# Performance work log

Hardware: AMD Instinct MI355X
Metric: run time of the kernel (lower is better)

The kernel has to match this reference:

```python
import jax, jax.numpy as jnp
import numpy as np

N_NODES = 100000
N_EDGES = 640000
IN_D = 128
OUT_D = 128


def setup_inputs() -> dict:
    key = jax.random.key(0)
    k_x, k_ei, k_ws, k_wn = jax.random.split(key, 4)
    scale = 1.0 / np.sqrt(IN_D)
    return {
        "x": jax.random.normal(k_x, (N_NODES, IN_D), dtype=jnp.float32),
        "ei": jax.random.randint(k_ei, (2, N_EDGES), 0, N_NODES, dtype=jnp.int64),
        "Ws": jax.random.normal(k_ws, (IN_D, OUT_D), dtype=jnp.float32) * scale,
        "bs": jnp.zeros((OUT_D,), dtype=jnp.float32),
        "Wn": jax.random.normal(k_wn, (IN_D, OUT_D), dtype=jnp.float32) * scale,
        "bn": jnp.zeros((OUT_D,), dtype=jnp.float32),
    }


def reference(x, ei, Ws, bs, Wn, bn):
    # x: [N, in_d], ei: [2, E]
    src, dst = ei[0], ei[1]
    n = x.shape[0]
    # scatter-sum of gathered source features onto destinations
    agg = jax.ops.segment_sum(x[src], dst, num_segments=n)  # [N, in_d]
    # in-degree per destination node
    deg = jax.ops.segment_sum(jnp.ones(src.shape[0], dtype=x.dtype), dst, num_segments=n)  # [N]
    agg = agg / jnp.maximum(deg, 1.0)[:, None]
    # dual linear + relu (dropout is identity in eval)
    return jax.nn.relu(x @ Ws + bs + agg @ Wn + bn)
```

## Files before the change

### kernel.cpp

```cpp
#include <hip/hip_runtime.h>
#include <hip/hip_bf16.h>

#define D 128

typedef __attribute__((ext_vector_type(8))) short short8v;
typedef __attribute__((ext_vector_type(4))) float f32x4;

__device__ __forceinline__ short f2bf(float f) {
    union { float f; unsigned u; } v;
    v.f = f;
    unsigned u = v.u;
    unsigned r = (u + 0x7FFFu + ((u >> 16) & 1u)) >> 16;
    return (short)r;
}

__device__ __forceinline__ float bf2f(unsigned u16) {
    union { unsigned u; float f; } v;
    v.u = u16 << 16;
    return v.f;
}

__device__ __forceinline__ unsigned pkbf2(float lo, float hi) {
    __hip_bfloat162 h = __float22bfloat162_rn(make_float2(lo, hi));
    union { __hip_bfloat162 h; unsigned u; } v;
    v.h = h;
    return v.u;
}

__global__ __launch_bounds__(256) void prep_kernel(const int* __restrict__ dst,
                                                   int* __restrict__ counts, int nE,
                                                   const float* __restrict__ Ws,
                                                   const float* __restrict__ Wn,
                                                   short* __restrict__ WT2,
                                                   const float* __restrict__ x,
                                                   unsigned short* __restrict__ xb,
                                                   int nElem) {
    const int nbE = (nE + 255) >> 8;
    const int b = blockIdx.x;
    if (b < nbE) {
        int e = b * 256 + threadIdx.x;
        if (e < nE) atomicAdd(&counts[dst[e]], 1);
    } else if (b < nbE + 128) {
        int idx = (b - nbE) * 256 + threadIdx.x;
        int nn = idx >> 8;
        int k = idx & 255;
        float v = (k < D) ? Ws[k * D + nn] : Wn[(k - D) * D + nn];
        WT2[idx] = f2bf(v);
    } else {
        int idx = (b - nbE - 128) * 256 + threadIdx.x;
        int base = idx * 8;
        if (base < nElem) {
            float4 lo = *reinterpret_cast<const float4*>(x + base);
            float4 hi = *reinterpret_cast<const float4*>(x + base + 4);
            union { short8v s8; unsigned u[4]; } p;
            p.u[0] = pkbf2(lo.x, lo.y);
            p.u[1] = pkbf2(lo.z, lo.w);
            p.u[2] = pkbf2(hi.x, hi.y);
            p.u[3] = pkbf2(hi.z, hi.w);
            *reinterpret_cast<short8v*>(xb + base) = p.s8;
        }
    }
}

__global__ __launch_bounds__(256) void scan_fused_kernel(int* __restrict__ counts,
                                                         int* __restrict__ bsums,
                                                         int* __restrict__ done,
                                                         int* __restrict__ rowptr,
                                                         int n, int nb) {
    __shared__ int sh[256];
    __shared__ int red[8];
    const int b = blockIdx.x;
    const int t = threadIdx.x;
    const int i0 = b * 1024 + t * 4;
    int c[4];
    int s = 0;
#pragma unroll
    for (int j = 0; j < 4; ++j) {
        c[j] = (i0 + j < n) ? counts[i0 + j] : 0;
        s += c[j];
    }
    sh[t] = s;
    __syncthreads();
    for (int off = 1; off < 256; off <<= 1) {
        int u = (t >= off) ? sh[t - off] : 0;
        __syncthreads();
        sh[t] += u;
        __syncthreads();
    }
    if (t == 0) {
        bsums[b] = sh[255];
        __threadfence();
        atomicAdd(done, 1);
        while (atomicAdd(done, 0) < nb) { }
    }
    __syncthreads();
    int xv = (t < nb) ? atomicAdd(&bsums[t], 0) : 0;
    int vb = (t < b) ? xv : 0;
#pragma unroll
    for (int off = 32; off > 0; off >>= 1) {
        vb += __shfl_down(vb, off, 64);
        xv += __shfl_down(xv, off, 64);
    }
    if ((t & 63) == 0) { red[t >> 6] = vb; red[4 + (t >> 6)] = xv; }
    __syncthreads();
    const int base = red[0] + red[1] + red[2] + red[3];
    const int total = red[4] + red[5] + red[6] + red[7];
    int run = base + sh[t] - s;
#pragma unroll
    for (int j = 0; j < 4; ++j) {
        int i = i0 + j;
        if (i < n) {
            rowptr[i] = run;
            counts[i] = run;
            run += c[j];
        }
    }
    if (b == nb - 1 && t == 0) rowptr[n] = total;
}

__global__ __launch_bounds__(256) void fill_kernel(const int* __restrict__ src,
                                                   const int* __restrict__ dst,
                                                   int* __restrict__ cursor,
                                                   int* __restrict__ csr, int nE) {
    int e = blockIdx.x * 256 + threadIdx.x;
    if (e < nE) {
        int pos = atomicAdd(&cursor[dst[e]], 1);
        csr[pos] = src[e];
    }
}

__global__ __launch_bounds__(256) void gather_kernel(const int* __restrict__ rowptr,
                                                     const int* __restrict__ csr,
                                                     const unsigned short* __restrict__ xb,
                                                     unsigned* __restrict__ aggOut,
                                                     int aggStride, int n) {
    const int wave = threadIdx.x >> 6;
    const int lane = threadIdx.x & 63;
    const int d0 = blockIdx.x * 8 + wave * 2;
    if (d0 >= n) return;
    const bool has1 = (d0 + 1) < n;

    const int begA = rowptr[d0];
    const int endA = rowptr[d0 + 1];
    const int begB = has1 ? endA : 0;
    const int endB = has1 ? rowptr[d0 + 2] : 0;
    const int ofs = lane * 2;
    float ax0 = 0.f, ay0 = 0.f, ax1 = 0.f, ay1 = 0.f;
    int iA = begA, iB = begB;

#define GLD(sidx) (*reinterpret_cast<const unsigned*>(xb + (size_t)(sidx) * D + ofs))
    while (iA + 4 <= endA && iB + 4 <= endB) {
        int a0 = csr[iA], a1 = csr[iA + 1], a2 = csr[iA + 2], a3 = csr[iA + 3];
        int b0 = csr[iB], b1 = csr[iB + 1], b2 = csr[iB + 2], b3 = csr[iB + 3];
        unsigned va0 = GLD(a0), va1 = GLD(a1), va2 = GLD(a2), va3 = GLD(a3);
        unsigned vb0 = GLD(b0), vb1 = GLD(b1), vb2 = GLD(b2), vb3 = GLD(b3);
        ax0 += (bf2f(va0 & 0xffffu) + bf2f(va1 & 0xffffu)) +
               (bf2f(va2 & 0xffffu) + bf2f(va3 & 0xffffu));
        ay0 += (bf2f(va0 >> 16) + bf2f(va1 >> 16)) + (bf2f(va2 >> 16) + bf2f(va3 >> 16));
        ax1 += (bf2f(vb0 & 0xffffu) + bf2f(vb1 & 0xffffu)) +
               (bf2f(vb2 & 0xffffu) + bf2f(vb3 & 0xffffu));
        ay1 += (bf2f(vb0 >> 16) + bf2f(vb1 >> 16)) + (bf2f(vb2 >> 16) + bf2f(vb3 >> 16));
        iA += 4;
        iB += 4;
    }
    while (iA + 4 <= endA) {
        int a0 = csr[iA], a1 = csr[iA + 1], a2 = csr[iA + 2], a3 = csr[iA + 3];
        unsigned va0 = GLD(a0), va1 = GLD(a1), va2 = GLD(a2), va3 = GLD(a3);
        ax0 += (bf2f(va0 & 0xffffu) + bf2f(va1 & 0xffffu)) +
               (bf2f(va2 & 0xffffu) + bf2f(va3 & 0xffffu));
        ay0 += (bf2f(va0 >> 16) + bf2f(va1 >> 16)) + (bf2f(va2 >> 16) + bf2f(va3 >> 16));
        iA += 4;
    }
    while (iB + 4 <= endB) {
        int b0 = csr[iB], b1 = csr[iB + 1], b2 = csr[iB + 2], b3 = csr[iB + 3];
        unsigned vb0 = GLD(b0), vb1 = GLD(b1), vb2 = GLD(b2), vb3 = GLD(b3);
        ax1 += (bf2f(vb0 & 0xffffu) + bf2f(vb1 & 0xffffu)) +
               (bf2f(vb2 & 0xffffu) + bf2f(vb3 & 0xffffu));
        ay1 += (bf2f(vb0 >> 16) + bf2f(vb1 >> 16)) + (bf2f(vb2 >> 16) + bf2f(vb3 >> 16));
        iB += 4;
    }
    while (iA < endA) {
        unsigned v = GLD(csr[iA]);
        ax0 += bf2f(v & 0xffffu);
        ay0 += bf2f(v >> 16);
        ++iA;
    }
    while (iB < endB) {
        unsigned v = GLD(csr[iB]);
        ax1 += bf2f(v & 0xffffu);
        ay1 += bf2f(v >> 16);
        ++iB;
    }
#undef GLD

    const float invA = 1.0f / fmaxf((float)(endA - begA), 1.0f);
    aggOut[(size_t)d0 * aggStride + lane] = pkbf2(ax0 * invA, ay0 * invA);
    if (has1) {
        const float invB = 1.0f / fmaxf((float)(endB - begB), 1.0f);
        aggOut[(size_t)(d0 + 1) * aggStride + lane] = pkbf2(ax1 * invB, ay1 * invB);
    }
}

template <bool INPLACE>
__global__ __launch_bounds__(256) void gemm_kernel(const unsigned short* __restrict__ xb,
                                                   const short* __restrict__ WT2,
                                                   const float* __restrict__ bs,
                                                   const float* __restrict__ bn,
                                                   const unsigned* aggIn, int aggStride,
                                                   float* __restrict__ out, int nStrips) {
    const int wave = threadIdx.x >> 6;
    const int lane = threadIdx.x & 63;
    const int lrow = lane & 15;
    const int q = lane >> 4;
    const int ko = q * 8;

    short8v b[2][8];
#pragma unroll
    for (int j = 0; j < 2; ++j) {
        const short* __restrict__ wp = WT2 + (size_t)((wave * 2 + j) * 16 + lrow) * 256 + ko;
#pragma unroll
        for (int ks = 0; ks < 8; ++ks)
            b[j][ks] = *reinterpret_cast<const short8v*>(wp + ks * 32);
    }
    float4 bias[2];
#pragma unroll
    for (int j = 0; j < 2; ++j) {
        const int cb = (wave * 2 + j) * 16 + q * 4;
        float4 v1 = *reinterpret_cast<const float4*>(bs + cb);
        float4 v2 = *reinterpret_cast<const float4*>(bn + cb);
        bias[j] = make_float4(v1.x + v2.x, v1.y + v2.y, v1.z + v2.z, v1.w + v2.w);
    }

    const int stride = gridDim.x;

    auto loadA = [&](int strip, short8v* ax, uint4* ag) {
        const unsigned short* __restrict__ xr = xb + (size_t)(strip * 16 + lrow) * D + ko;
        const unsigned* __restrict__ ar = aggIn + (size_t)(strip * 16 + lrow) * aggStride;
#pragma unroll
        for (int ks = 0; ks < 4; ++ks) {
            ax[ks] = *reinterpret_cast<const short8v*>(xr + ks * 32);
            ag[ks] = *reinterpret_cast<const uint4*>(ar + q * 4 + ks * 16);
        }
    };

    auto compute = [&](int strip, const short8v* ax, const uint4* ag) {
        f32x4 acc[2];
        acc[0] = (f32x4){0.f, 0.f, 0.f, 0.f};
        acc[1] = (f32x4){0.f, 0.f, 0.f, 0.f};
#pragma unroll
        for (int j = 0; j < 2; ++j) {
#pragma unroll
            for (int ks = 0; ks < 4; ++ks) {
                union { uint4 u4; short8v s8; } cv;
                cv.u4 = ag[ks];
                acc[j] = __builtin_amdgcn_mfma_f32_16x16x32_bf16(b[j][ks], ax[ks], acc[j], 0, 0, 0);
                acc[j] = __builtin_amdgcn_mfma_f32_16x16x32_bf16(b[j][ks + 4], cv.s8, acc[j], 0, 0, 0);
            }
        }
        if (INPLACE) __syncthreads();
        const size_t rb = (size_t)(strip * 16 + lrow) * D;
#pragma unroll
        for (int j = 0; j < 2; ++j) {
            const int cb = (wave * 2 + j) * 16 + q * 4;
            float4 o;
            o.x = fmaxf(acc[j][0] + bias[j].x, 0.f);
            o.y = fmaxf(acc[j][1] + bias[j].y, 0.f);
            o.z = fmaxf(acc[j][2] + bias[j].z, 0.f);
            o.w = fmaxf(acc[j][3] + bias[j].w, 0.f);
            *reinterpret_cast<float4*>(out + rb + cb) = o;
        }
    };

    short8v axA[4], axB[4];
    uint4 agA[4], agB[4];
    int strip = blockIdx.x;
    if (strip >= nStrips) return;
    loadA(strip, axA, agA);
    for (; strip < nStrips; strip += 2 * stride) {
        const int s1 = strip + stride;
        if (s1 < nStrips) loadA(s1, axB, agB);
        compute(strip, axA, agA);
        if (s1 < nStrips) {
            const int s2 = s1 + stride;
            if (s2 < nStrips) loadA(s2, axA, agA);
            compute(s1, axB, agB);
        }
    }
}

extern "C" void kernel_launch(void* const* d_in, const int* in_sizes, int n_in,
                              void* d_out, int out_size, void* d_ws, size_t ws_size,
                              hipStream_t stream) {
    const float* x  = (const float*)d_in[0];
    const int*   ei = (const int*)d_in[1];
    const float* Ws = (const float*)d_in[2];
    const float* bs = (const float*)d_in[3];
    const float* Wn = (const float*)d_in[4];
    const float* bn = (const float*)d_in[5];
    float* out = (float*)d_out;

    const int n  = in_sizes[0] / D;
    const int nE = in_sizes[1] / 2;
    const int* src = ei;
    const int* dst = ei + nE;
    const int nb = (n + 1023) / 1024;
    const int nElem = n * D;

    char* w = (char*)d_ws;
    unsigned short* xb = (unsigned short*)w;  w += (size_t)nElem * 2;
    short* WT2   = (short*)w;                 w += (size_t)256 * D * 2;
    int* counts  = (int*)w;                   w += (size_t)n * 4;
    int* bsums   = (int*)w;                   w += 128 * 4;
    int* done    = (int*)w;                   w += 16;
    int* rowptr  = (int*)w;                   w += (size_t)(n + 1) * 4;
    int* csr     = (int*)w;                   w += (size_t)nE * 4;
    size_t off = (size_t)(w - (char*)d_ws);
    off = (off + 15) & ~(size_t)15;
    unsigned short* aggb = (unsigned short*)((char*)d_ws + off);
    const bool sep = (off + (size_t)nElem * 2) <= ws_size;

    const int nbE = (nE + 255) / 256;
    const int nXb = (nElem / 8 + 255) / 256;

    hipMemsetAsync(counts, 0, (size_t)(n + 128 + 4) * sizeof(int), stream);
    prep_kernel<<<nbE + 128 + nXb, 256, 0, stream>>>(dst, counts, nE, Ws, Wn, WT2, x, xb, nElem);
    scan_fused_kernel<<<nb, 256, 0, stream>>>(counts, bsums, done, rowptr, n, nb);
    fill_kernel<<<(nE + 255) / 256, 256, 0, stream>>>(src, dst, counts, csr, nE);

    unsigned* aggPtr = sep ? (unsigned*)aggb : (unsigned*)out;
    const int aggStride = sep ? (D / 2) : D;
    gather_kernel<<<(n + 7) / 8, 256, 0, stream>>>(rowptr, csr, xb, aggPtr, aggStride, n);

    const int nStrips = (n + 15) / 16;
    if (sep)
        gemm_kernel<false><<<2048, 256, 0, stream>>>(xb, WT2, bs, bn, (const unsigned*)aggb,
                                                     aggStride, out, nStrips);
    else
        gemm_kernel<true><<<2048, 256, 0, stream>>>(xb, WT2, bs, bn, (const unsigned*)out,
                                                    aggStride, out, nStrips);
}
```

Measured before the change: 163.2 us.

## Fuse CSR fill into scan kernel via grid barrier, nontemporal output, fewer GEMM blocks

Merges the fill kernel into the scan kernel using a spin-wait grid barrier on the done counter, removing one launch and its dependency gap. The fill loop is grid-strided over the scan's roughly 98 blocks, so it has much less parallelism than the old fill launch. The GEMM epilogue now uses nontemporal stores to avoid polluting the cache with output, and the GEMM grid is halved. The spin barrier assumes all scan blocks are co-resident, which holds at this block count.

```diff
diff --git a/kernel.cpp b/kernel.cpp
--- a/kernel.cpp
+++ b/kernel.cpp
@@ -62,11 +62,14 @@
     }
 }
 
-__global__ __launch_bounds__(256) void scan_fused_kernel(int* __restrict__ counts,
-                                                         int* __restrict__ bsums,
-                                                         int* __restrict__ done,
-                                                         int* __restrict__ rowptr,
-                                                         int n, int nb) {
+__global__ __launch_bounds__(256) void scan_fill_kernel(int* __restrict__ counts,
+                                                        int* __restrict__ bsums,
+                                                        int* __restrict__ done,
+                                                        int* __restrict__ rowptr,
+                                                        const int* __restrict__ src,
+                                                        const int* __restrict__ dst,
+                                                        int* __restrict__ csr, int nE,
+                                                        int n, int nb) {
     __shared__ int sh[256];
     __shared__ int red[8];
     const int b = blockIdx.x;
@@ -111,20 +114,22 @@
         int i = i0 + j;
         if (i < n) {
             rowptr[i] = run;
-            counts[i] = run;
+            atomicExch(&counts[i], run);
             run += c[j];
         }
     }
     if (b == nb - 1 && t == 0) rowptr[n] = total;
-}
-
-__global__ __launch_bounds__(256) void fill_kernel(const int* __restrict__ src,
-                                                   const int* __restrict__ dst,
-                                                   int* __restrict__ cursor,
-                                                   int* __restrict__ csr, int nE) {
-    int e = blockIdx.x * 256 + threadIdx.x;
-    if (e < nE) {
-        int pos = atomicAdd(&cursor[dst[e]], 1);
+
+    __syncthreads();
+    if (t == 0) {
+        atomicAdd(done, 1);
+        while (atomicAdd(done, 0) < 2 * nb) { }
+    }
+    __syncthreads();
+
+    const int gsz = nb * 256;
+    for (int e = b * 256 + t; e < nE; e += gsz) {
+        int pos = atomicAdd(&counts[dst[e]], 1);
         csr[pos] = src[e];
     }
 }
@@ -262,12 +267,12 @@
 #pragma unroll
         for (int j = 0; j < 2; ++j) {
             const int cb = (wave * 2 + j) * 16 + q * 4;
-            float4 o;
-            o.x = fmaxf(acc[j][0] + bias[j].x, 0.f);
-            o.y = fmaxf(acc[j][1] + bias[j].y, 0.f);
-            o.z = fmaxf(acc[j][2] + bias[j].z, 0.f);
-            o.w = fmaxf(acc[j][3] + bias[j].w, 0.f);
-            *reinterpret_cast<float4*>(out + rb + cb) = o;
+            f32x4 o;
+            o[0] = fmaxf(acc[j][0] + bias[j].x, 0.f);
+            o[1] = fmaxf(acc[j][1] + bias[j].y, 0.f);
+            o[2] = fmaxf(acc[j][2] + bias[j].z, 0.f);
+            o[3] = fmaxf(acc[j][3] + bias[j].w, 0.f);
+            __builtin_nontemporal_store(o, reinterpret_cast<f32x4*>(out + rb + cb));
         }
     };
 
@@ -322,10 +327,9 @@
     const int nbE = (nE + 255) / 256;
     const int nXb = (nElem / 8 + 255) / 256;
 
-    hipMemsetAsync(counts, 0, (size_t)(n + 128 + 4) * sizeof(int), stream);
+    (void)hipMemsetAsync(counts, 0, (size_t)(n + 128 + 4) * sizeof(int), stream);
     prep_kernel<<<nbE + 128 + nXb, 256, 0, stream>>>(dst, counts, nE, Ws, Wn, WT2, x, xb, nElem);
-    scan_fused_kernel<<<nb, 256, 0, stream>>>(counts, bsums, done, rowptr, n, nb);
-    fill_kernel<<<(nE + 255) / 256, 256, 0, stream>>>(src, dst, counts, csr, nE);
+    scan_fill_kernel<<<nb, 256, 0, stream>>>(counts, bsums, done, rowptr, src, dst, csr, nE, n, nb);
 
     unsigned* aggPtr = sep ? (unsigned*)aggb : (unsigned*)out;
     const int aggStride = sep ? (D / 2) : D;
@@ -333,9 +337,9 @@
 
     const int nStrips = (n + 15) / 16;
     if (sep)
-        gemm_kernel<false><<<2048, 256, 0, stream>>>(xb, WT2, bs, bn, (const unsigned*)aggb,
+        gemm_kernel<false><<<1024, 256, 0, stream>>>(xb, WT2, bs, bn, (const unsigned*)aggb,
                                                      aggStride, out, nStrips);
     else
-        gemm_kernel<true><<<2048, 256, 0, stream>>>(xb, WT2, bs, bn, (const unsigned*)out,
+        gemm_kernel<true><<<1024, 256, 0, stream>>>(xb, WT2, bs, bn, (const unsigned*)out,
                                                     aggStride, out, nStrips);
 }
```

Result: faster. 158.1 us (-3.1%).
